# Performance work log

Hardware: AMD Instinct MI355X
Metric: run time of the kernel (lower is better)

## Reference

```python
import jax, jax.numpy as jnp
import numpy as np

D_MODEL = 1024
NUM_HEADS = 16
D_K = D_MODEL // NUM_HEADS
BATCH = 4
SEQ = 2048


def setup_inputs() -> dict:
    key = jax.random.key(0)
    ks = jax.random.split(key, 16)
    s = 0.02
    return {
        "query": jax.random.normal(ks[0], (BATCH, SEQ, D_MODEL), jnp.float32),
        "key": jax.random.normal(ks[1], (BATCH, SEQ, D_MODEL), jnp.float32),
        "value": jax.random.normal(ks[2], (BATCH, SEQ, D_MODEL), jnp.float32),
        "Wq": jax.random.normal(ks[3], (D_MODEL, D_MODEL), jnp.float32) * s,
        "bq": jnp.zeros((D_MODEL,), jnp.float32),
        "Wk": jax.random.normal(ks[4], (D_MODEL, D_MODEL), jnp.float32) * s,
        "bk": jnp.zeros((D_MODEL,), jnp.float32),
        "Wv": jax.random.normal(ks[5], (D_MODEL, D_MODEL), jnp.float32) * s,
        "bv": jnp.zeros((D_MODEL,), jnp.float32),
        "Wo": jax.random.normal(ks[6], (D_MODEL, D_MODEL), jnp.float32) * s,
        "bo": jnp.zeros((D_MODEL,), jnp.float32),
        "gamma": jnp.ones((D_MODEL,), jnp.float32),
        "beta": jnp.zeros((D_MODEL,), jnp.float32),
    }


def _layer_norm(x, gamma, beta, eps=1e-5):
    mu = jnp.mean(x, axis=-1, keepdims=True)
    var = jnp.var(x, axis=-1, keepdims=True)
    return (x - mu) * jax.lax.rsqrt(var + eps) * gamma + beta


def reference(query, key, value, Wq, bq, Wk, bk, Wv, bv, Wo, bo, gamma, beta):
    B, S, _ = query.shape
    residual = query
    # projections -> [B, H, S, d_k]
    Q = (query @ Wq + bq).reshape(B, S, NUM_HEADS, D_K).transpose(0, 2, 1, 3)
    K = (key @ Wk + bk).reshape(B, -1, NUM_HEADS, D_K).transpose(0, 2, 1, 3)
    V = (value @ Wv + bv).reshape(B, -1, NUM_HEADS, D_K).transpose(0, 2, 1, 3)
    scale = 1.0 / jnp.sqrt(jnp.asarray(D_K, query.dtype))
    scores = jnp.einsum("bhqd,bhkd->bhqk", Q, K) * scale  # [B,H,S,S]
    attn = jax.nn.softmax(scores, axis=-1)
    ctx = jnp.einsum("bhqk,bhkd->bhqd", attn, V)
    ctx = ctx.transpose(0, 2, 1, 3).reshape(B, S, D_MODEL)
    out = ctx @ Wo + bo
    return _layer_norm(residual + out, gamma, beta)
```

## Files before the change

kernel.cpp:

```cpp
#include <hip/hip_runtime.h>

#define D_MODEL 1024
#define NUM_HEADS 16
#define DK 64
#define BATCH 4
#define SEQ 2048
#define MTOT (BATCH*SEQ)

typedef __attribute__((ext_vector_type(8))) short short8;
typedef __attribute__((ext_vector_type(4))) float f32x4;
typedef __attribute__((ext_vector_type(4))) unsigned int u32x4;

__device__ __forceinline__ unsigned short f2bf(float f) {
    union { float f; unsigned u; } v; v.f = f;
    unsigned r = v.u + 0x7FFFu + ((v.u >> 16) & 1u);
    return (unsigned short)(r >> 16);
}

__device__ __forceinline__ unsigned cvtpk(float lo, float hi) {
    unsigned r;
    asm("v_cvt_pk_bf16_f32 %0, %1, %2" : "=v"(r) : "v"(lo), "v"(hi));
    return r;
}

__device__ __forceinline__ void gload16(const unsigned short* g, unsigned short* l) {
    __builtin_amdgcn_global_load_lds(
        (const __attribute__((address_space(1))) unsigned int*)g,
        (__attribute__((address_space(3))) unsigned int*)l, 16, 0, 0);
}

__global__ __launch_bounds__(256) void mha_wtrans4(
    const float* __restrict__ W0, const float* __restrict__ W1,
    const float* __restrict__ W2, const float* __restrict__ W3,
    unsigned short* __restrict__ T0, unsigned short* __restrict__ T1,
    unsigned short* __restrict__ T2, unsigned short* __restrict__ T3) {
    __shared__ float tile[64][65];
    int z = blockIdx.z;
    const float* W = z == 0 ? W0 : z == 1 ? W1 : z == 2 ? W2 : W3;
    unsigned short* WT = z == 0 ? T0 : z == 1 ? T1 : z == 2 ? T2 : T3;
    int n0 = blockIdx.x * 64, k0 = blockIdx.y * 64;
    int tx = threadIdx.x & 63, ty = threadIdx.x >> 6;
#pragma unroll
    for (int i = 0; i < 16; ++i)
        tile[ty + i * 4][tx] = W[(size_t)(k0 + ty + i * 4) * D_MODEL + n0 + tx];
    __syncthreads();
#pragma unroll
    for (int i = 0; i < 16; ++i)
        WT[(size_t)(n0 + ty + i * 4) * D_MODEL + k0 + tx] = f2bf(tile[tx][ty + i * 4]);
}

__device__ __forceinline__ void stageB(const unsigned short* Bg, unsigned short* Bl,
                                       int wid, int rsub, int c8, int kk, int bcol) {
#pragma unroll
    for (int q = 0; q < 4; ++q) {
        int i = wid * 4 + q;
        int row = i * 8 + rsub;
        int gcol = kk + ((c8 ^ (row & 7)) << 3);
        gload16(Bg + (size_t)(bcol + row) * D_MODEL + gcol, Bl + i * 512);
    }
}

__device__ __forceinline__ void gemm_compute(const unsigned short* Al, const unsigned short* Bl,
                                             f32x4 (&acc)[4][4],
                                             int wr, int wc, int l15, int lg, int l7) {
    short8 af[4][2], bf[4][2];
#pragma unroll
    for (int mi = 0; mi < 4; ++mi)
#pragma unroll
        for (int ks = 0; ks < 2; ++ks)
            af[mi][ks] = *reinterpret_cast<const short8*>(
                &Al[(wr * 64 + mi * 16 + l15) * 64 + (((ks * 4 + lg) ^ l7) << 3)]);
#pragma unroll
    for (int ni = 0; ni < 4; ++ni)
#pragma unroll
        for (int ks = 0; ks < 2; ++ks)
            bf[ni][ks] = *reinterpret_cast<const short8*>(
                &Bl[(wc * 64 + ni * 16 + l15) * 64 + (((ks * 4 + lg) ^ l7) << 3)]);
#pragma unroll
    for (int mi = 0; mi < 4; ++mi)
#pragma unroll
        for (int ni = 0; ni < 4; ++ni)
#pragma unroll
            for (int ks = 0; ks < 2; ++ks)
                acc[mi][ni] = __builtin_amdgcn_mfma_f32_16x16x32_bf16(
                    af[mi][ks], bf[ni][ks], acc[mi][ni], 0, 0, 0);
}

__global__ __launch_bounds__(256) void mha_gemm_qkvc(
    const float* __restrict__ Aqf, const float* __restrict__ Akf,
    const float* __restrict__ Avf,
    const unsigned short* __restrict__ Wq, const unsigned short* __restrict__ Wk,
    const unsigned short* __restrict__ Wv,
    const float* __restrict__ bq, const float* __restrict__ bk, const float* __restrict__ bv,
    unsigned short* __restrict__ Qb, unsigned short* __restrict__ Kb,
    unsigned short* __restrict__ VT, float qscale) {
    __shared__ unsigned short SM[32768];
    unsigned short* A0 = SM;
    unsigned short* B0 = SM + 8192;
    unsigned short* A1 = SM + 16384;
    unsigned short* B1 = SM + 24576;

    int z = blockIdx.z;
    const float* A = z == 0 ? Aqf : z == 1 ? Akf : Avf;
    const unsigned short* WT = z == 0 ? Wq : z == 1 ? Wk : Wv;
    const float* bias = z == 0 ? bq : z == 1 ? bk : bv;

    int wid = threadIdx.x >> 6;
    int lane = threadIdx.x & 63;
    int wr = wid >> 1, wc = wid & 1;
    int brow = blockIdx.x * 128;
    int bcol = blockIdx.y * 128;
    int l15 = lane & 15, lg = lane >> 4;
    int c8 = lane & 7, rsub = lane >> 3;
    int l7 = l15 & 7;

    int arow[4], acol[4];
#pragma unroll
    for (int q = 0; q < 4; ++q) {
        int i = wid * 4 + q;
        int row = i * 8 + rsub;
        arow[q] = row;
        acol[q] = (c8 ^ (row & 7)) << 3;
    }

#define ALOAD(rA, kk)                                                            \
    do {                                                                         \
        _Pragma("unroll")                                                        \
        for (int q = 0; q < 4; ++q) {                                            \
            const float* ap = A + (size_t)(brow + arow[q]) * D_MODEL + (kk) + acol[q]; \
            rA[q][0] = *reinterpret_cast<const float4*>(ap);                     \
            rA[q][1] = *reinterpret_cast<const float4*>(ap + 4);                 \
        }                                                                        \
    } while (0)

#define AWRITE(rA, Al)                                                           \
    do {                                                                         \
        _Pragma("unroll")                                                        \
        for (int q = 0; q < 4; ++q) {                                            \
            int i = wid * 4 + q;                                                 \
            u32x4 u = (u32x4){cvtpk(rA[q][0].x, rA[q][0].y),                     \
                              cvtpk(rA[q][0].z, rA[q][0].w),                     \
                              cvtpk(rA[q][1].x, rA[q][1].y),                     \
                              cvtpk(rA[q][1].z, rA[q][1].w)};                    \
            *reinterpret_cast<u32x4*>(Al + i * 512 + rsub * 64 + c8 * 8) = u;    \
        }                                                                        \
    } while (0)

    f32x4 acc[4][4] = {};
    {
        float4 r0[4][2];
        ALOAD(r0, 0);
        stageB(WT, B0, wid, rsub, c8, 0, bcol);
        AWRITE(r0, A0);
        __syncthreads();
    }
    for (int kk = 0; kk < D_MODEL; kk += 128) {
        float4 rB[4][2];
        ALOAD(rB, kk + 64);
        stageB(WT, B1, wid, rsub, c8, kk + 64, bcol);
        gemm_compute(A0, B0, acc, wr, wc, l15, lg, l7);
        AWRITE(rB, A1);
        __syncthreads();
        bool more = (kk + 128) < D_MODEL;
        float4 rC[4][2];
        if (more) {
            ALOAD(rC, kk + 128);
            stageB(WT, B0, wid, rsub, c8, kk + 128, bcol);
        }
        gemm_compute(A1, B1, acc, wr, wc, l15, lg, l7);
        if (more) AWRITE(rC, A0);
        __syncthreads();
    }
#undef ALOAD
#undef AWRITE

    if (z < 2) {
        unsigned short* outb = z == 0 ? Qb : Kb;
        float scale = z == 0 ? qscale : 1.0f;
#pragma unroll
        for (int ni = 0; ni < 4; ++ni) {
            int col = bcol + wc * 64 + ni * 16 + l15;
            float bv2 = bias[col];
#pragma unroll
            for (int mi = 0; mi < 4; ++mi)
#pragma unroll
                for (int j = 0; j < 4; ++j) {
                    int row = brow + wr * 64 + mi * 16 + lg * 4 + j;
                    outb[(size_t)row * D_MODEL + col] = f2bf((acc[mi][ni][j] + bv2) * scale);
                }
        }
    } else {
        unsigned short* T = SM;
#pragma unroll
        for (int ni = 0; ni < 4; ++ni) {
            int c = wc * 64 + ni * 16 + l15;
            float bv2 = bias[bcol + c];
#pragma unroll
            for (int mi = 0; mi < 4; ++mi)
#pragma unroll
                for (int j = 0; j < 4; ++j) {
                    int r = wr * 64 + mi * 16 + lg * 4 + j;
                    T[c * 136 + r] = f2bf(acc[mi][ni][j] + bv2);
                }
        }
        __syncthreads();
        int c = threadIdx.x >> 1;
        int rh = (threadIdx.x & 1) * 64;
        int gcol = bcol + c;
        int h = gcol >> 6, d = gcol & 63;
        int b = brow >> 11, s0 = brow & (SEQ - 1);
        unsigned short* dst = VT + ((size_t)((b * 16 + h) * 64 + d)) * SEQ + s0 + rh;
        const unsigned short* src = &T[c * 136 + rh];
#pragma unroll
        for (int i = 0; i < 8; ++i)
            *reinterpret_cast<short8*>(dst + i * 8) =
                *reinterpret_cast<const short8*>(src + i * 8);
    }
}

__device__ __forceinline__ void gemm_stage(const unsigned short* Ag, const unsigned short* Bg,
                                           unsigned short* Al, unsigned short* Bl,
                                           int wid, int rsub, int c8, int kk,
                                           int brow, int bcol) {
#pragma unroll
    for (int q = 0; q < 4; ++q) {
        int i = wid * 4 + q;
        int row = i * 8 + rsub;
        int gcol = kk + ((c8 ^ (row & 7)) << 3);
        gload16(Ag + (size_t)(brow + row) * D_MODEL + gcol, Al + i * 512);
        gload16(Bg + (size_t)(bcol + row) * D_MODEL + gcol, Bl + i * 512);
    }
}

__global__ __launch_bounds__(256) void mha_gemm_o(const unsigned short* __restrict__ A,
                                                  const unsigned short* __restrict__ WT,
                                                  const float* __restrict__ bias,
                                                  const float* __restrict__ residual,
                                                  float* __restrict__ outf) {
    __shared__ unsigned short SM[32768];
    unsigned short* A0 = SM;
    unsigned short* B0 = SM + 8192;
    unsigned short* A1 = SM + 16384;
    unsigned short* B1 = SM + 24576;

    int wid = threadIdx.x >> 6;
    int lane = threadIdx.x & 63;
    int wr = wid >> 1, wc = wid & 1;
    int brow = blockIdx.x * 128;
    int bcol = blockIdx.y * 128;
    int l15 = lane & 15, lg = lane >> 4;
    int c8 = lane & 7, rsub = lane >> 3;
    int l7 = l15 & 7;

    f32x4 acc[4][4] = {};
    gemm_stage(A, WT, A0, B0, wid, rsub, c8, 0, brow, bcol);
    __syncthreads();
    for (int kk = 0; kk < D_MODEL; kk += 128) {
        gemm_stage(A, WT, A1, B1, wid, rsub, c8, kk + 64, brow, bcol);
        gemm_compute(A0, B0, acc, wr, wc, l15, lg, l7);
        __syncthreads();
        if (kk + 128 < D_MODEL)
            gemm_stage(A, WT, A0, B0, wid, rsub, c8, kk + 128, brow, bcol);
        gemm_compute(A1, B1, acc, wr, wc, l15, lg, l7);
        __syncthreads();
    }
#pragma unroll
    for (int ni = 0; ni < 4; ++ni) {
        int col = bcol + wc * 64 + ni * 16 + l15;
        float bv2 = bias[col];
#pragma unroll
        for (int mi = 0; mi < 4; ++mi)
#pragma unroll
            for (int j = 0; j < 4; ++j) {
                int row = brow + wr * 64 + mi * 16 + lg * 4 + j;
                outf[(size_t)row * D_MODEL + col] =
                    acc[mi][ni][j] + bv2 + residual[(size_t)row * D_MODEL + col];
            }
    }
}

__device__ __forceinline__ void attn_tile(const unsigned short* Kd,
                                          const unsigned short* Vd,
                                          const short8 aq[2][2],
                                          f32x4 (&acc)[2][4],
                                          float (&lsum)[2],
                                          int l15, int lg, int l7) {
    f32x4 z[2][4];
#pragma unroll
    for (int t = 0; t < 4; ++t) {
        int krow = (t * 16 + l15) * 64;
        short8 kf0 = *reinterpret_cast<const short8*>(&Kd[krow + ((lg ^ l7) << 3)]);
        short8 kf1 = *reinterpret_cast<const short8*>(&Kd[krow + (((4 + lg) ^ l7) << 3)]);
#pragma unroll
        for (int m = 0; m < 2; ++m) {
            f32x4 zz = {};
            zz = __builtin_amdgcn_mfma_f32_16x16x32_bf16(kf0, aq[m][0], zz, 0, 0, 0);
            zz = __builtin_amdgcn_mfma_f32_16x16x32_bf16(kf1, aq[m][1], zz, 0, 0, 0);
            z[m][t] = zz;
        }
    }
#pragma unroll
    for (int m = 0; m < 2; ++m)
#pragma unroll
        for (int t = 0; t < 4; ++t)
#pragma unroll
            for (int j = 0; j < 4; ++j) {
                float p = __builtin_amdgcn_exp2f(z[m][t][j]);
                z[m][t][j] = p;
                lsum[m] += p;
            }
    short8 pf[2][2];
#pragma unroll
    for (int m = 0; m < 2; ++m)
#pragma unroll
        for (int ks = 0; ks < 2; ++ks) {
            union { u32x4 u; short8 s; } cv;
            cv.u = (u32x4){cvtpk(z[m][2 * ks][0], z[m][2 * ks][1]),
                           cvtpk(z[m][2 * ks][2], z[m][2 * ks][3]),
                           cvtpk(z[m][2 * ks + 1][0], z[m][2 * ks + 1][1]),
                           cvtpk(z[m][2 * ks + 1][2], z[m][2 * ks + 1][3])};
            pf[m][ks] = cv.s;
        }
#pragma unroll
    for (int dt = 0; dt < 4; ++dt) {
        int vrow = (dt * 16 + l15) * 64;
        short8 vf0 = *reinterpret_cast<const short8*>(&Vd[vrow + ((lg ^ l7) << 3)]);
        short8 vf1 = *reinterpret_cast<const short8*>(&Vd[vrow + (((4 + lg) ^ l7) << 3)]);
#pragma unroll
        for (int m = 0; m < 2; ++m) {
            acc[m][dt] = __builtin_amdgcn_mfma_f32_16x16x32_bf16(vf0, pf[m][0], acc[m][dt], 0, 0, 0);
            acc[m][dt] = __builtin_amdgcn_mfma_f32_16x16x32_bf16(vf1, pf[m][1], acc[m][dt], 0, 0, 0);
        }
    }
}

__global__ __launch_bounds__(256, 4) void mha_attn(const unsigned short* __restrict__ Q,
                                                   const unsigned short* __restrict__ K,
                                                   const unsigned short* __restrict__ VT,
                                                   unsigned short* __restrict__ ctx) {
    __shared__ unsigned short K0[64 * 64], V0[64 * 64];
    __shared__ unsigned short K1[64 * 64], V1[64 * 64];

    int lane = threadIdx.x & 63;
    int w = threadIdx.x >> 6;
    int l15 = lane & 15, lg = lane >> 4;
    int l7 = l15 & 7;
    int c8 = lane & 7, rsub = lane >> 3;

    int id = blockIdx.x + gridDim.x * blockIdx.y;
    int nid = (id & 7) * 128 + (id >> 3);
    int bx = nid & 15;
    int bh = nid >> 4;
    int b = bh >> 4, h = bh & 15;
    int q0 = bx * 128 + w * 32;

    short8 aq[2][2];
    {
        const unsigned short* Qp = Q + (size_t)(b * SEQ + q0) * D_MODEL + h * DK;
#pragma unroll
        for (int m = 0; m < 2; ++m)
#pragma unroll
            for (int ks = 0; ks < 2; ++ks)
                aq[m][ks] = *reinterpret_cast<const short8*>(
                    Qp + (size_t)(m * 16 + l15) * D_MODEL + ks * 32 + lg * 8);
    }

    f32x4 acc[2][4] = {};
    float lsum[2] = {};

    const unsigned short* Kbh = K + (size_t)(b * SEQ) * D_MODEL + h * DK;
    const unsigned short* VTbh = VT + (size_t)bh * DK * SEQ;

    int i0 = w * 2, i1 = w * 2 + 1;
    int row0 = i0 * 8 + rsub, row1 = i1 * 8 + rsub;
    int sw0 = (c8 ^ (row0 & 7)) << 3, sw1 = (c8 ^ (row1 & 7)) << 3;
    int sr0 = (row0 & 32) | ((row0 & 12) << 1) | ((row0 & 16) >> 2) | (row0 & 3);
    int sr1 = (row1 & 32) | ((row1 & 12) << 1) | ((row1 & 16) >> 2) | (row1 & 3);

#define STAGE(Kd, Vd, kb)                                                        \
    do {                                                                         \
        gload16(Kbh + (size_t)((kb) + sr0) * D_MODEL + sw0, (Kd) + i0 * 512);    \
        gload16(Kbh + (size_t)((kb) + sr1) * D_MODEL + sw1, (Kd) + i1 * 512);    \
        gload16(VTbh + (size_t)row0 * SEQ + (kb) + sw0, (Vd) + i0 * 512);        \
        gload16(VTbh + (size_t)row1 * SEQ + (kb) + sw1, (Vd) + i1 * 512);        \
    } while (0)

    STAGE(K0, V0, 0);
    __syncthreads();

    for (int kb = 0; kb < SEQ; kb += 128) {
        STAGE(K1, V1, kb + 64);
        attn_tile(K0, V0, aq, acc, lsum, l15, lg, l7);
        __syncthreads();
        if (kb + 128 < SEQ) STAGE(K0, V0, kb + 128);
        attn_tile(K1, V1, aq, acc, lsum, l15, lg, l7);
        __syncthreads();
    }
#undef STAGE

#pragma unroll
    for (int m = 0; m < 2; ++m) {
        float l = lsum[m];
        l += __shfl_xor(l, 16);
        l += __shfl_xor(l, 32);
        float rl = 1.0f / l;
        int q = q0 + m * 16 + l15;
        unsigned short* cp = ctx + (size_t)(b * SEQ + q) * D_MODEL + h * DK + lg * 4;
#pragma unroll
        for (int dt = 0; dt < 4; ++dt) {
            ushort4 o;
            o.x = f2bf(acc[m][dt][0] * rl);
            o.y = f2bf(acc[m][dt][1] * rl);
            o.z = f2bf(acc[m][dt][2] * rl);
            o.w = f2bf(acc[m][dt][3] * rl);
            *reinterpret_cast<ushort4*>(cp + dt * 16) = o;
        }
    }
}

__global__ __launch_bounds__(256) void mha_ln(const float* __restrict__ X,
                                              const float* __restrict__ gamma,
                                              const float* __restrict__ beta,
                                              float* __restrict__ out) {
    int row = blockIdx.x;
    int t = threadIdx.x;
    const float* x = X + (size_t)row * D_MODEL;
    float4 v = reinterpret_cast<const float4*>(x)[t];
    float s = v.x + v.y + v.z + v.w;
    float s2 = v.x * v.x + v.y * v.y + v.z * v.z + v.w * v.w;
#pragma unroll
    for (int off = 1; off < 64; off <<= 1) {
        s += __shfl_xor(s, off);
        s2 += __shfl_xor(s2, off);
    }
    __shared__ float ws[8];
    int wid = t >> 6;
    if ((t & 63) == 0) { ws[wid] = s; ws[4 + wid] = s2; }
    __syncthreads();
    s = ws[0] + ws[1] + ws[2] + ws[3];
    s2 = ws[4] + ws[5] + ws[6] + ws[7];
    float mu = s * (1.f / D_MODEL);
    float var = s2 * (1.f / D_MODEL) - mu * mu;
    float rstd = rsqrtf(var + 1e-5f);
    float4 gv = reinterpret_cast<const float4*>(gamma)[t];
    float4 bv = reinterpret_cast<const float4*>(beta)[t];
    float4 o;
    o.x = (v.x - mu) * rstd * gv.x + bv.x;
    o.y = (v.y - mu) * rstd * gv.y + bv.y;
    o.z = (v.z - mu) * rstd * gv.z + bv.z;
    o.w = (v.w - mu) * rstd * gv.w + bv.w;
    reinterpret_cast<float4*>(out + (size_t)row * D_MODEL)[t] = o;
}

extern "C" void kernel_launch(void* const* d_in, const int* in_sizes, int n_in,
                              void* d_out, int out_size, void* d_ws, size_t ws_size,
                              hipStream_t stream) {
    const float* query = (const float*)d_in[0];
    const float* key   = (const float*)d_in[1];
    const float* value = (const float*)d_in[2];
    const float* Wq = (const float*)d_in[3];
    const float* bq = (const float*)d_in[4];
    const float* Wk = (const float*)d_in[5];
    const float* bk = (const float*)d_in[6];
    const float* Wv = (const float*)d_in[7];
    const float* bv = (const float*)d_in[8];
    const float* Wo = (const float*)d_in[9];
    const float* bo = (const float*)d_in[10];
    const float* gamma = (const float*)d_in[11];
    const float* beta  = (const float*)d_in[12];

    char* ws = (char*)d_ws;
    const size_t MB = 1u << 20;
    unsigned short* WTq = (unsigned short*)(ws + 0 * MB);
    unsigned short* WTk = (unsigned short*)(ws + 2 * MB);
    unsigned short* WTv = (unsigned short*)(ws + 4 * MB);
    unsigned short* WTo = (unsigned short*)(ws + 6 * MB);
    unsigned short* Qb  = (unsigned short*)(ws + 8 * MB);
    unsigned short* Kb  = (unsigned short*)(ws + 25 * MB);
    unsigned short* VT  = (unsigned short*)(ws + 42 * MB);
    unsigned short* ctx = (unsigned short*)(ws + 59 * MB);
    float* tmp          = (float*)(ws + 8 * MB);

    const float C1 = 0.180336880f;

    dim3 b256(256);
    mha_wtrans4<<<dim3(16, 16, 4), b256, 0, stream>>>(Wq, Wk, Wv, Wo, WTq, WTk, WTv, WTo);

    mha_gemm_qkvc<<<dim3(MTOT / 128, D_MODEL / 128, 3), b256, 0, stream>>>(
        query, key, value, WTq, WTk, WTv, bq, bk, bv, Qb, Kb, VT, C1);

    mha_attn<<<dim3(SEQ / 128, BATCH * NUM_HEADS), b256, 0, stream>>>(Qb, Kb, VT, ctx);

    mha_gemm_o<<<dim3(MTOT / 128, D_MODEL / 128), b256, 0, stream>>>(ctx, WTo, bo, query, tmp);

    mha_ln<<<dim3(MTOT), b256, 0, stream>>>(tmp, gamma, beta, (float*)d_out);
}
```

Measured before the change: 198.0 us.

## Replace double-buffered LDS staging with single buffer in projection GEMMs

```diff
diff --git a/kernel.cpp b/kernel.cpp
--- a/kernel.cpp
+++ b/kernel.cpp
@@ -94,11 +94,9 @@
     const float* __restrict__ bq, const float* __restrict__ bk, const float* __restrict__ bv,
     unsigned short* __restrict__ Qb, unsigned short* __restrict__ Kb,
     unsigned short* __restrict__ VT, float qscale) {
-    __shared__ unsigned short SM[32768];
-    unsigned short* A0 = SM;
-    unsigned short* B0 = SM + 8192;
-    unsigned short* A1 = SM + 16384;
-    unsigned short* B1 = SM + 24576;
+    __shared__ unsigned short SM[17408];
+    unsigned short* Al = SM;
+    unsigned short* Bl = SM + 8192;
 
     int z = blockIdx.z;
     const float* A = z == 0 ? Aqf : z == 1 ? Akf : Avf;
@@ -133,7 +131,7 @@
         }                                                                        \
     } while (0)
 
-#define AWRITE(rA, Al)                                                           \
+#define AWRITE(rA)                                                               \
     do {                                                                         \
         _Pragma("unroll")                                                        \
         for (int q = 0; q < 4; ++q) {                                            \
@@ -147,29 +145,15 @@
     } while (0)
 
     f32x4 acc[4][4] = {};
-    {
-        float4 r0[4][2];
-        ALOAD(r0, 0);
-        stageB(WT, B0, wid, rsub, c8, 0, bcol);
-        AWRITE(r0, A0);
-        __syncthreads();
-    }
-    for (int kk = 0; kk < D_MODEL; kk += 128) {
-        float4 rB[4][2];
-        ALOAD(rB, kk + 64);
-        stageB(WT, B1, wid, rsub, c8, kk + 64, bcol);
-        gemm_compute(A0, B0, acc, wr, wc, l15, lg, l7);
-        AWRITE(rB, A1);
-        __syncthreads();
-        bool more = (kk + 128) < D_MODEL;
-        float4 rC[4][2];
-        if (more) {
-            ALOAD(rC, kk + 128);
-            stageB(WT, B0, wid, rsub, c8, kk + 128, bcol);
-        }
-        gemm_compute(A1, B1, acc, wr, wc, l15, lg, l7);
-        if (more) AWRITE(rC, A0);
-        __syncthreads();
+    float4 rA[4][2];
+    ALOAD(rA, 0);
+    for (int kk = 0; kk < D_MODEL; kk += 64) {
+        __syncthreads();
+        stageB(WT, Bl, wid, rsub, c8, kk, bcol);
+        AWRITE(rA);
+        __syncthreads();
+        if (kk + 64 < D_MODEL) ALOAD(rA, kk + 64);
+        gemm_compute(Al, Bl, acc, wr, wc, l15, lg, l7);
     }
 #undef ALOAD
 #undef AWRITE
@@ -190,6 +174,7 @@
                 }
         }
     } else {
+        __syncthreads();
         unsigned short* T = SM;
 #pragma unroll
         for (int ni = 0; ni < 4; ++ni) {
@@ -237,11 +222,9 @@
                                                   const float* __restrict__ bias,
                                                   const float* __restrict__ residual,
                                                   float* __restrict__ outf) {
-    __shared__ unsigned short SM[32768];
-    unsigned short* A0 = SM;
-    unsigned short* B0 = SM + 8192;
-    unsigned short* A1 = SM + 16384;
-    unsigned short* B1 = SM + 24576;
+    __shared__ unsigned short SM[16384];
+    unsigned short* Al = SM;
+    unsigned short* Bl = SM + 8192;
 
     int wid = threadIdx.x >> 6;
     int lane = threadIdx.x & 63;
@@ -253,16 +236,11 @@
     int l7 = l15 & 7;
 
     f32x4 acc[4][4] = {};
-    gemm_stage(A, WT, A0, B0, wid, rsub, c8, 0, brow, bcol);
-    __syncthreads();
-    for (int kk = 0; kk < D_MODEL; kk += 128) {
-        gemm_stage(A, WT, A1, B1, wid, rsub, c8, kk + 64, brow, bcol);
-        gemm_compute(A0, B0, acc, wr, wc, l15, lg, l7);
-        __syncthreads();
-        if (kk + 128 < D_MODEL)
-            gemm_stage(A, WT, A0, B0, wid, rsub, c8, kk + 128, brow, bcol);
-        gemm_compute(A1, B1, acc, wr, wc, l15, lg, l7);
-        __syncthreads();
+    for (int kk = 0; kk < D_MODEL; kk += 64) {
+        __syncthreads();
+        gemm_stage(A, WT, Al, Bl, wid, rsub, c8, kk, brow, bcol);
+        __syncthreads();
+        gemm_compute(Al, Bl, acc, wr, wc, l15, lg, l7);
     }
 #pragma unroll
     for (int ni = 0; ni < 4; ++ni) {
```

Measured after the change: 200.2 us. Within noise of the previous version (+1.1%).
